# Kernel tuning notes

Hardware: AMD Instinct MI355X
Metric: run time of the kernel (lower is better)

Reference implementation:

```python
import jax, jax.numpy as jnp
import numpy as np
from jax import lax

GRID_SIZE = 5
SPLINE_ORDER = 3
N_COEF = GRID_SIZE + SPLINE_ORDER  # 8 b-spline basis functions per input
GRID_LO, GRID_HI = -1.0, 1.0


def _grid():
    h = (GRID_HI - GRID_LO) / GRID_SIZE
    return jnp.arange(-SPLINE_ORDER, GRID_SIZE + SPLINE_ORDER + 1, dtype=jnp.float32) * h + GRID_LO


def _bsplines(x):
    # x: [..., in] -> [..., in, N_COEF] via Cox-de Boor recursion (efficient-kan)
    grid = _grid()
    x = x[..., None]
    bases = ((x >= grid[:-1]) & (x < grid[1:])).astype(x.dtype)
    for j in range(1, SPLINE_ORDER + 1):
        bases = ((x - grid[:-(j + 1)]) / (grid[j:-1] - grid[:-(j + 1)]) * bases[..., :-1]
                 + (grid[j + 1:] - x) / (grid[j + 1:] - grid[1:-j]) * bases[..., 1:])
    return bases


def _kan_linear(x, base_w, spline_w):
    # x: [..., in]; base_w: [out, in]; spline_w: [out, in, N_COEF]
    base = jax.nn.silu(x) @ base_w.T
    b = _bsplines(x).reshape(x.shape[:-1] + (-1,))  # [..., in*N_COEF]
    return base + b @ spline_w.reshape(spline_w.shape[0], -1).T


def _kan_conv(x, base_w, spline_w):
    # x: [B, C, H, W]; 3x3 valid KAN convolution
    patches = lax.conv_general_dilated_patches(x, (3, 3), (1, 1), 'VALID')  # [B, C*9, H-2, W-2]
    p = patches.transpose(0, 2, 3, 1)  # [B, Ho, Wo, C*9]
    out = _kan_linear(p, base_w, spline_w)  # [B, Ho, Wo, out]
    return out.transpose(0, 3, 1, 2)


def _maxpool2(x):
    return lax.reduce_window(x, -jnp.inf, lax.max, (1, 1, 2, 2), (1, 1, 2, 2), 'VALID')


def setup_inputs() -> dict:
    key = jax.random.key(0)
    ks = jax.random.split(key, 12)
    B = 2048
    x = jax.random.uniform(ks[0], (B, 1, 28, 28), dtype=jnp.float32)
    s = 0.1
    return {
        'x': x,
        'bw1': jax.random.normal(ks[1], (5, 9), dtype=jnp.float32) * s,
        'sw1': jax.random.normal(ks[2], (5, 9, N_COEF), dtype=jnp.float32) * s,
        'bw2': jax.random.normal(ks[3], (5, 45), dtype=jnp.float32) * s,
        'sw2': jax.random.normal(ks[4], (5, 45, N_COEF), dtype=jnp.float32) * s,
        'bw3': jax.random.normal(ks[5], (2, 45), dtype=jnp.float32) * s,
        'sw3': jax.random.normal(ks[6], (2, 45, N_COEF), dtype=jnp.float32) * s,
        'w1': jax.random.normal(ks[7], (500, 162), dtype=jnp.float32) * 0.05,
        'b1': jnp.zeros((500,), dtype=jnp.float32),
        'w2': jax.random.normal(ks[8], (10, 500), dtype=jnp.float32) * 0.05,
        'b2': jnp.zeros((10,), dtype=jnp.float32),
    }


def reference(x, bw1, sw1, bw2, sw2, bw3, sw3, w1, b1, w2, b2):
    h = _kan_conv(x, bw1, sw1)       # [B, 5, 26, 26]
    h = _maxpool2(h)                 # [B, 5, 13, 13]
    h = _kan_conv(h, bw2, sw2)       # [B, 5, 11, 11]
    h = _kan_conv(h, bw3, sw3)       # [B, 2, 9, 9]
    h = h.reshape(h.shape[0], -1)    # [B, 162]
    h = jax.nn.relu(h @ w1.T + b1)   # [B, 500]
    return h @ w2.T + b2             # [B, 10]
```

## Files before the change

kernel.cpp:

```cpp
#include <hip/hip_runtime.h>


typedef _Float16 h2 __attribute__((ext_vector_type(2)));

__device__ __forceinline__ h2 u2h(unsigned int u) {
  union { unsigned int x; h2 h; } v; v.x = u; return v.h;
}
__device__ __forceinline__ unsigned short f2h_bits(float x) {
  union { _Float16 h; unsigned short u; } v; v.h = (_Float16)x; return v.u;
}
__device__ __forceinline__ float h2f(unsigned short u) {
  union { unsigned short u; _Float16 h; } v; v.u = u; return (float)v.h;
}
__device__ __forceinline__ unsigned int pack2h(float a, float b) {
  return (unsigned int)f2h_bits(a) | ((unsigned int)f2h_bits(b) << 16);
}
__device__ __forceinline__ float fdot2(h2 a, h2 b, float c) {
  return __builtin_amdgcn_fdot2(a, b, c, false);
}

__device__ __forceinline__ void featurize_regs(float v, uint4& bs, float& silu) {
  silu = v / (1.0f + __expf(-v));
  bs.x = 0u; bs.y = 0u; bs.z = 0u; bs.w = 0u;
  float u = fmaf(v, 2.5f, 5.5f);
  if (u >= 0.0f && u < 11.0f) {
    float tf = floorf(u);
    float f = u - tf, f2 = f * f, f3 = f2 * f, om = 1.0f - f;
    const float c6 = 1.0f / 6.0f;
    float w0 = om * om * om * c6;
    float w1 = (3.0f * f3 - 6.0f * f2 + 4.0f) * c6;
    float w2 = (-3.0f * f3 + 3.0f * f2 + 3.0f * f + 1.0f) * c6;
    float w3 = f3 * c6;
    unsigned long long w01 =
        (unsigned long long)f2h_bits(w0) |
        ((unsigned long long)f2h_bits(w1) << 16) |
        ((unsigned long long)f2h_bits(w2) << 32) |
        ((unsigned long long)f2h_bits(w3) << 48);
    int t = (int)tf;
    int s = 16 * t - 48;
    unsigned long long lo, hi;
    if (s >= 0) {
      lo = (s < 64) ? (w01 << s) : 0ull;
      hi = (s == 0) ? 0ull : ((s < 64) ? (w01 >> (64 - s)) : (w01 << (s - 64)));
    } else {
      lo = w01 >> (-s);
      hi = 0ull;
    }
    bs.x = (unsigned int)lo; bs.y = (unsigned int)(lo >> 32);
    bs.z = (unsigned int)hi; bs.w = (unsigned int)(hi >> 32);
  }
}

template <int OB, int NO>
__device__ __forceinline__ void conv2_accum(
    const uint4* bas, const unsigned short* slu16,
    const unsigned int* __restrict__ V2s, const float* __restrict__ V2b,
    int y0, int x0, float (&acc)[NO]) {
  #pragma unroll 1
  for (int cky = 0; cky < 15; ++cky) {
    int c = cky / 3, ky = cky - c * 3;
    int ba0 = c * 169 + (y0 + ky) * 13 + x0;
    uint4 q00 = bas[ba0], q01 = bas[ba0 + 1], q02 = bas[ba0 + 2];
    float s00 = h2f(slu16[ba0]), s01 = h2f(slu16[ba0 + 1]), s02 = h2f(slu16[ba0 + 2]);
    uint4 wq[3 * NO]; float wb[3 * NO];
    const uint4* wp4 = (const uint4*)(V2s + cky * 60);
    const float* bp  = V2b + cky * 15;
    #pragma unroll
    for (int kx = 0; kx < 3; ++kx)
      #pragma unroll
      for (int j = 0; j < NO; ++j) {
        wq[kx * NO + j] = wp4[kx * 5 + OB + j];
        wb[kx * NO + j] = bp[kx * 5 + OB + j];
      }
    #pragma unroll
    for (int kx = 0; kx < 3; ++kx) {
      uint4 q = (kx == 0) ? q00 : ((kx == 1) ? q01 : q02);
      float sl = (kx == 0) ? s00 : ((kx == 1) ? s01 : s02);
      h2 a0 = u2h(q.x), a1 = u2h(q.y), a2 = u2h(q.z), a3 = u2h(q.w);
      #pragma unroll
      for (int j = 0; j < NO; ++j) {
        uint4 w = wq[kx * NO + j];
        float a = acc[j];
        a = fdot2(a0, u2h(w.x), a);
        a = fdot2(a1, u2h(w.y), a);
        a = fdot2(a2, u2h(w.z), a);
        a = fdot2(a3, u2h(w.w), a);
        acc[j] = fmaf(sl, wb[kx * NO + j], a);
      }
    }
  }
}

__global__ __launch_bounds__(256) void k_prep(
    const float* __restrict__ bw1, const float* __restrict__ sw1,
    const float* __restrict__ bw2, const float* __restrict__ sw2,
    const float* __restrict__ bw3, const float* __restrict__ sw3,
    const float* __restrict__ w1, const float* __restrict__ w2,
    unsigned int* __restrict__ V1s, float* __restrict__ V1b,
    unsigned int* __restrict__ V2s, float* __restrict__ V2b,
    unsigned int* __restrict__ V3s, float* __restrict__ V3b,
    unsigned int* __restrict__ W1p4, float* __restrict__ W2p) {
  int t = blockIdx.x * 256 + threadIdx.x;
  if (t < 180) {
    int p = t & 3, o = (t >> 2) % 5, in = t / 20;
    V1s[t] = pack2h(sw1[(o * 9 + in) * 8 + 2 * p], sw1[(o * 9 + in) * 8 + 2 * p + 1]);
  }
  if (t < 45)  { int o = t % 5, in = t / 5; V1b[t] = bw1[o * 9 + in]; }
  if (t < 900) {
    int p = t & 3, o = (t >> 2) % 5, in = t / 20;
    V2s[t] = pack2h(sw2[(o * 45 + in) * 8 + 2 * p], sw2[(o * 45 + in) * 8 + 2 * p + 1]);
  }
  if (t < 225) { int o = t % 5, in = t / 5; V2b[t] = bw2[o * 45 + in]; }
  if (t < 360) {
    int p = t & 3, o = (t >> 2) & 1, in = t / 8;
    V3s[t] = pack2h(sw3[(o * 45 + in) * 8 + 2 * p], sw3[(o * 45 + in) * 8 + 2 * p + 1]);
  }
  if (t < 90)  { int o = t % 2, in = t / 2; V3b[t] = bw3[o * 45 + in]; }
  if (t < 43008) {
    int j = t & 3, o = (t >> 2) & 511, g = t >> 11;
    int kp = g * 4 + j;
    W1p4[t] = (o < 500 && kp < 81)
                  ? pack2h(w1[o * 162 + 2 * kp], w1[o * 162 + 2 * kp + 1])
                  : 0u;
  }
  if (t < 5120) {
    int o = t >> 9, k = t & 511;
    W2p[t] = (k < 500) ? w2[o * 500 + k] : 0.0f;
  }
}

__global__ __launch_bounds__(256, 8) void k_fused(
    const float* __restrict__ x,
    const unsigned int* __restrict__ V1s, const float* __restrict__ V1b,
    const unsigned int* __restrict__ V2s, const float* __restrict__ V2b,
    const unsigned int* __restrict__ V3s, const float* __restrict__ V3b,
    const unsigned int* __restrict__ W1p4, const float* __restrict__ W2p,
    const float* __restrict__ b1, const float* __restrict__ b2,
    float* __restrict__ out) {
  __shared__ uint4 bas[845];
  __shared__ unsigned short slu16[848];
  __shared__ float red[40];
  float*        basF = (float*)bas;
  float*        h3f  = basF + 2048;
  unsigned int* hpk  = (unsigned int*)basF + 2560;
  const int b = blockIdx.x;
  const int tid = threadIdx.x;

  #pragma unroll 1
  for (int l = tid; l < 784; l += 256) {
    uint4 bs; float sl;
    featurize_regs(x[b * 784 + l], bs, sl);
    bas[l] = bs; slu16[l] = f2h_bits(sl);
  }
  __syncthreads();

  float h1v[5];
  if (tid < 169) {
    int py = tid / 13, px = tid % 13;
    int r0 = py * 2, c0 = px * 2;
    float wacc[4][5];
    #pragma unroll
    for (int wi = 0; wi < 4; ++wi)
      #pragma unroll
      for (int o = 0; o < 5; ++o) wacc[wi][o] = 0.0f;
    #pragma unroll
    for (int r = 0; r < 4; ++r) {
      uint4 q[4]; float sl[4];
      #pragma unroll
      for (int c = 0; c < 4; ++c) {
        q[c]  = bas[(r0 + r) * 28 + c0 + c];
        sl[c] = h2f(slu16[(r0 + r) * 28 + c0 + c]);
      }
      #pragma unroll
      for (int c = 0; c < 4; ++c) {
        h2 a0 = u2h(q[c].x), a1 = u2h(q[c].y), a2 = u2h(q[c].z), a3 = u2h(q[c].w);
        #pragma unroll
        for (int dy = 0; dy < 2; ++dy) {
          #pragma unroll
          for (int dx = 0; dx < 2; ++dx) {
            int ky = r - dy, kx = c - dx;
            if (ky >= 0 && ky < 3 && kx >= 0 && kx < 3) {
              const unsigned int* wp = V1s + (ky * 3 + kx) * 20;
              const float* bp = V1b + (ky * 3 + kx) * 5;
              #pragma unroll
              for (int o = 0; o < 5; ++o) {
                float acc = wacc[dy * 2 + dx][o];
                acc = fdot2(a0, u2h(wp[o * 4 + 0]), acc);
                acc = fdot2(a1, u2h(wp[o * 4 + 1]), acc);
                acc = fdot2(a2, u2h(wp[o * 4 + 2]), acc);
                acc = fdot2(a3, u2h(wp[o * 4 + 3]), acc);
                wacc[dy * 2 + dx][o] = fmaf(sl[c], bp[o], acc);
              }
            }
          }
        }
      }
    }
    #pragma unroll
    for (int o = 0; o < 5; ++o)
      h1v[o] = fmaxf(fmaxf(wacc[0][o], wacc[1][o]),
                     fmaxf(wacc[2][o], wacc[3][o]));
  }
  __syncthreads();
  if (tid < 169) {
    #pragma unroll
    for (int o = 0; o < 5; ++o) {
      uint4 bs; float sl;
      featurize_regs(h1v[o], bs, sl);
      bas[o * 169 + tid] = bs; slu16[o * 169 + tid] = f2h_bits(sl);
    }
  }
  __syncthreads();

  int og = __builtin_amdgcn_readfirstlane(tid >> 7);
  int p2 = tid & 127;
  float acc2a[3] = {0.0f, 0.0f, 0.0f};
  float acc2b[2] = {0.0f, 0.0f};
  {
    int pc = (p2 < 121) ? p2 : 120;
    int y0 = pc / 11, x0 = pc % 11;
    if (og == 0) conv2_accum<0, 3>(bas, slu16, V2s, V2b, y0, x0, acc2a);
    else         conv2_accum<3, 2>(bas, slu16, V2s, V2b, y0, x0, acc2b);
  }
  __syncthreads();
  if (p2 < 121) {
    if (og == 0) {
      #pragma unroll
      for (int j = 0; j < 3; ++j) {
        uint4 bs; float sl;
        featurize_regs(acc2a[j], bs, sl);
        bas[j * 121 + p2] = bs; slu16[j * 121 + p2] = f2h_bits(sl);
      }
    } else {
      #pragma unroll
      for (int j = 0; j < 2; ++j) {
        uint4 bs; float sl;
        featurize_regs(acc2b[j], bs, sl);
        bas[(3 + j) * 121 + p2] = bs; slu16[(3 + j) * 121 + p2] = f2h_bits(sl);
      }
    }
  }
  __syncthreads();

  float acc3 = 0.0f;
  {
    int ou = og;
    int pc = (p2 < 81) ? p2 : 80;
    int y0 = pc / 9, x0 = pc % 9;
    #pragma unroll 1
    for (int cky = 0; cky < 15; ++cky) {
      int c = cky / 3, ky = cky - c * 3;
      int ba0 = c * 121 + (y0 + ky) * 11 + x0;
      uint4 q00 = bas[ba0], q01 = bas[ba0 + 1], q02 = bas[ba0 + 2];
      float s00 = h2f(slu16[ba0]), s01 = h2f(slu16[ba0 + 1]), s02 = h2f(slu16[ba0 + 2]);
      uint4 wq[3]; float wb[3];
      const uint4* wp4 = (const uint4*)(V3s + cky * 24);
      const float* bp  = V3b + cky * 6;
      #pragma unroll
      for (int kx = 0; kx < 3; ++kx) {
        wq[kx] = wp4[kx * 2 + ou];
        wb[kx] = bp[kx * 2 + ou];
      }
      #pragma unroll
      for (int kx = 0; kx < 3; ++kx) {
        uint4 q = (kx == 0) ? q00 : ((kx == 1) ? q01 : q02);
        float sl = (kx == 0) ? s00 : ((kx == 1) ? s01 : s02);
        h2 a0 = u2h(q.x), a1 = u2h(q.y), a2 = u2h(q.z), a3 = u2h(q.w);
        uint4 w = wq[kx];
        float a = acc3;
        a = fdot2(a0, u2h(w.x), a);
        a = fdot2(a1, u2h(w.y), a);
        a = fdot2(a2, u2h(w.z), a);
        a = fdot2(a3, u2h(w.w), a);
        acc3 = fmaf(sl, wb[kx], a);
      }
    }
  }
  __syncthreads();
  if (p2 < 81) h3f[og * 81 + p2] = acc3;
  __syncthreads();
  if (tid < 84)
    hpk[tid] = (tid < 81) ? pack2h(h3f[2 * tid], h3f[2 * tid + 1]) : 0u;
  __syncthreads();

  float fa[2] = {0.0f, 0.0f};
  {
    const uint4* hp4 = (const uint4*)hpk;
    const uint4* wbase = (const uint4*)W1p4 + tid;
    uint4 wA[2], wB[2];
    #pragma unroll
    for (int i = 0; i < 2; ++i) wA[i] = wbase[i * 256];
    #pragma unroll 1
    for (int g = 0; g < 21; g += 2) {
      if (g + 1 < 21) {
        const uint4* p = wbase + (g + 1) * 512;
        #pragma unroll
        for (int i = 0; i < 2; ++i) wB[i] = p[i * 256];
      }
      {
        uint4 hk = hp4[g];
        #pragma unroll
        for (int i = 0; i < 2; ++i) {
          float a = fa[i];
          a = fdot2(u2h(hk.x), u2h(wA[i].x), a);
          a = fdot2(u2h(hk.y), u2h(wA[i].y), a);
          a = fdot2(u2h(hk.z), u2h(wA[i].z), a);
          a = fdot2(u2h(hk.w), u2h(wA[i].w), a);
          fa[i] = a;
        }
      }
      if (g + 2 < 21) {
        const uint4* p = wbase + (g + 2) * 512;
        #pragma unroll
        for (int i = 0; i < 2; ++i) wA[i] = p[i * 256];
      }
      if (g + 1 < 21) {
        uint4 hk = hp4[g + 1];
        #pragma unroll
        for (int i = 0; i < 2; ++i) {
          float a = fa[i];
          a = fdot2(u2h(hk.x), u2h(wB[i].x), a);
          a = fdot2(u2h(hk.y), u2h(wB[i].y), a);
          a = fdot2(u2h(hk.z), u2h(wB[i].z), a);
          a = fdot2(u2h(hk.w), u2h(wB[i].w), a);
          fa[i] = a;
        }
      }
    }
  }
  #pragma unroll
  for (int i = 0; i < 2; ++i) {
    int o = tid + 256 * i;
    float bb = (o < 500) ? b1[o] : 0.0f;
    float v = fa[i] + bb;
    basF[o] = (v > 0.0f && o < 500) ? v : 0.0f;
  }
  __syncthreads();

  float acc10[10];
  {
    float2 ha = ((const float2*)basF)[tid];
    #pragma unroll
    for (int o = 0; o < 10; ++o) {
      float2 w = ((const float2*)&W2p[o * 512])[tid];
      acc10[o] = ha.x * w.x + ha.y * w.y;
    }
  }
  #pragma unroll
  for (int off = 32; off > 0; off >>= 1) {
    #pragma unroll
    for (int o = 0; o < 10; ++o) acc10[o] += __shfl_down(acc10[o], off);
  }
  if ((tid & 63) == 0) {
    int wid = tid >> 6;
    #pragma unroll
    for (int o = 0; o < 10; ++o) red[wid * 10 + o] = acc10[o];
  }
  __syncthreads();
  if (tid < 10)
    out[b * 10 + tid] = red[tid] + red[10 + tid] + red[20 + tid] + red[30 + tid] + b2[tid];
}

extern "C" void kernel_launch(void* const* d_in, const int* in_sizes, int n_in,
                              void* d_out, int out_size, void* d_ws, size_t ws_size,
                              hipStream_t stream) {
  (void)in_sizes; (void)n_in; (void)out_size; (void)ws_size;
  const float* x   = (const float*)d_in[0];
  const float* bw1 = (const float*)d_in[1];
  const float* sw1 = (const float*)d_in[2];
  const float* bw2 = (const float*)d_in[3];
  const float* sw2 = (const float*)d_in[4];
  const float* bw3 = (const float*)d_in[5];
  const float* sw3 = (const float*)d_in[6];
  const float* w1  = (const float*)d_in[7];
  const float* b1  = (const float*)d_in[8];
  const float* w2  = (const float*)d_in[9];
  const float* b2  = (const float*)d_in[10];
  float* out = (float*)d_out;

  char* ws = (char*)d_ws;
  unsigned int* V1s  = (unsigned int*)(ws);
  float*        V1b  = (float*)(ws + 768);
  unsigned int* V2s  = (unsigned int*)(ws + 1024);
  float*        V2b  = (float*)(ws + 4672);
  unsigned int* V3s  = (unsigned int*)(ws + 5632);
  float*        V3b  = (float*)(ws + 7168);
  float*        W2p  = (float*)(ws + 7680);
  unsigned int* W1p4 = (unsigned int*)(ws + 28672);

  k_prep<<<168, 256, 0, stream>>>(bw1, sw1, bw2, sw2, bw3, sw3, w1, w2,
                                  V1s, V1b, V2s, V2b, V3s, V3b, W1p4, W2p);
  k_fused<<<2048, 256, 0, stream>>>(x, V1s, V1b, V2s, V2b, V3s, V3b,
                                    W1p4, W2p, b1, b2, out);
}
```

Measured before the change: 129.1 us.

## Process two images per block and stage KAN conv weights in LDS

Each block now handles two images with 512 threads, and the conv weight tables for all three KAN layers are copied once per block into shared memory. Inner loops then read them from LDS instead of global/scalar memory. The first-layer feature map is stored with even and odd columns split apart, so each pool thread's four column reads are contiguous, likely to cut bank conflicts. Weight loads in conv2 and conv3 are moved inside the kx loop to lower register pressure. In exchange, shared memory per block roughly doubles, which may limit occupancy. Launch bounds of 512 with 8 blocks per CU also constrain registers.

```diff
diff --git a/kernel.cpp b/kernel.cpp
--- a/kernel.cpp
+++ b/kernel.cpp
@@ -54,7 +54,7 @@
 template <int OB, int NO>
 __device__ __forceinline__ void conv2_accum(
     const uint4* bas, const unsigned short* slu16,
-    const unsigned int* __restrict__ V2s, const float* __restrict__ V2b,
+    const unsigned int* wV2s, const float* wV2b,
     int y0, int x0, float (&acc)[NO]) {
   #pragma unroll 1
   for (int cky = 0; cky < 15; ++cky) {
@@ -62,30 +62,28 @@
     int ba0 = c * 169 + (y0 + ky) * 13 + x0;
     uint4 q00 = bas[ba0], q01 = bas[ba0 + 1], q02 = bas[ba0 + 2];
     float s00 = h2f(slu16[ba0]), s01 = h2f(slu16[ba0 + 1]), s02 = h2f(slu16[ba0 + 2]);
-    uint4 wq[3 * NO]; float wb[3 * NO];
-    const uint4* wp4 = (const uint4*)(V2s + cky * 60);
-    const float* bp  = V2b + cky * 15;
-    #pragma unroll
-    for (int kx = 0; kx < 3; ++kx)
+    const uint4* wp4 = (const uint4*)(wV2s + cky * 60);
+    const float* bp  = wV2b + cky * 15;
+    #pragma unroll
+    for (int kx = 0; kx < 3; ++kx) {
+      uint4 wq[NO]; float wb[NO];
       #pragma unroll
       for (int j = 0; j < NO; ++j) {
-        wq[kx * NO + j] = wp4[kx * 5 + OB + j];
-        wb[kx * NO + j] = bp[kx * 5 + OB + j];
-      }
-    #pragma unroll
-    for (int kx = 0; kx < 3; ++kx) {
+        wq[j] = wp4[kx * 5 + OB + j];
+        wb[j] = bp[kx * 5 + OB + j];
+      }
       uint4 q = (kx == 0) ? q00 : ((kx == 1) ? q01 : q02);
       float sl = (kx == 0) ? s00 : ((kx == 1) ? s01 : s02);
       h2 a0 = u2h(q.x), a1 = u2h(q.y), a2 = u2h(q.z), a3 = u2h(q.w);
       #pragma unroll
       for (int j = 0; j < NO; ++j) {
-        uint4 w = wq[kx * NO + j];
+        uint4 w = wq[j];
         float a = acc[j];
         a = fdot2(a0, u2h(w.x), a);
         a = fdot2(a1, u2h(w.y), a);
         a = fdot2(a2, u2h(w.z), a);
         a = fdot2(a3, u2h(w.w), a);
-        acc[j] = fmaf(sl, wb[kx * NO + j], a);
+        acc[j] = fmaf(sl, wb[j], a);
       }
     }
   }
@@ -129,7 +127,7 @@
   }
 }
 
-__global__ __launch_bounds__(256, 8) void k_fused(
+__global__ __launch_bounds__(512, 8) void k_fused(
     const float* __restrict__ x,
     const unsigned int* __restrict__ V1s, const float* __restrict__ V1b,
     const unsigned int* __restrict__ V2s, const float* __restrict__ V2b,
@@ -137,27 +135,49 @@
     const unsigned int* __restrict__ W1p4, const float* __restrict__ W2p,
     const float* __restrict__ b1, const float* __restrict__ b2,
     float* __restrict__ out) {
-  __shared__ uint4 bas[845];
-  __shared__ unsigned short slu16[848];
-  __shared__ float red[40];
-  float*        basF = (float*)bas;
-  float*        h3f  = basF + 2048;
-  unsigned int* hpk  = (unsigned int*)basF + 2560;
-  const int b = blockIdx.x;
+  __shared__ uint4 bas[2][845];
+  __shared__ unsigned short slu16[2][848];
+  __shared__ float red[2][40];
+  __shared__ __align__(16) unsigned int wV1s[180];
+  __shared__ float wV1b[45];
+  __shared__ __align__(16) unsigned int wV2s[900];
+  __shared__ float wV2b[225];
+  __shared__ __align__(16) unsigned int wV3s[360];
+  __shared__ float wV3b[90];
+
   const int tid = threadIdx.x;
+  const int h   = tid >> 8;
+  const int t   = tid & 255;
+
+  uint4*          bas_h = bas[h];
+  unsigned short* slu_h = slu16[h];
+  float*          basF  = (float*)bas_h;
+  float*          h3f   = basF + 2048;
+  unsigned int*   hpk   = (unsigned int*)basF + 2560;
+  const int img = blockIdx.x * 2 + h;
+
+  if (tid < 180) wV1s[tid] = V1s[tid];
+  if (tid < 45)  wV1b[tid] = V1b[tid];
+  #pragma unroll
+  for (int i = tid; i < 900; i += 512) wV2s[i] = V2s[i];
+  if (tid < 225) wV2b[tid] = V2b[tid];
+  if (tid < 360) wV3s[tid] = V3s[tid];
+  if (tid < 90)  wV3b[tid] = V3b[tid];
 
   #pragma unroll 1
-  for (int l = tid; l < 784; l += 256) {
+  for (int l = t; l < 784; l += 256) {
     uint4 bs; float sl;
-    featurize_regs(x[b * 784 + l], bs, sl);
-    bas[l] = bs; slu16[l] = f2h_bits(sl);
+    featurize_regs(x[img * 784 + l], bs, sl);
+    int y = l / 28, xx = l - y * 28;
+    int idx = y * 28 + ((xx & 1) ? 14 : 0) + (xx >> 1);
+    bas_h[idx] = bs; slu_h[idx] = f2h_bits(sl);
   }
   __syncthreads();
 
   float h1v[5];
-  if (tid < 169) {
-    int py = tid / 13, px = tid % 13;
-    int r0 = py * 2, c0 = px * 2;
+  if (t < 169) {
+    int py = t / 13, px = t % 13;
+    int r0 = py * 2;
     float wacc[4][5];
     #pragma unroll
     for (int wi = 0; wi < 4; ++wi)
@@ -168,8 +188,9 @@
       uint4 q[4]; float sl[4];
       #pragma unroll
       for (int c = 0; c < 4; ++c) {
-        q[c]  = bas[(r0 + r) * 28 + c0 + c];
-        sl[c] = h2f(slu16[(r0 + r) * 28 + c0 + c]);
+        int idx = (r0 + r) * 28 + ((c & 1) ? 14 : 0) + px + (c >> 1);
+        q[c]  = bas_h[idx];
+        sl[c] = h2f(slu_h[idx]);
       }
       #pragma unroll
       for (int c = 0; c < 4; ++c) {
@@ -180,15 +201,16 @@
           for (int dx = 0; dx < 2; ++dx) {
             int ky = r - dy, kx = c - dx;
             if (ky >= 0 && ky < 3 && kx >= 0 && kx < 3) {
-              const unsigned int* wp = V1s + (ky * 3 + kx) * 20;
-              const float* bp = V1b + (ky * 3 + kx) * 5;
+              const uint4* wp4 = (const uint4*)(wV1s + (ky * 3 + kx) * 20);
+              const float* bp  = wV1b + (ky * 3 + kx) * 5;
               #pragma unroll
               for (int o = 0; o < 5; ++o) {
+                uint4 w = wp4[o];
                 float acc = wacc[dy * 2 + dx][o];
-                acc = fdot2(a0, u2h(wp[o * 4 + 0]), acc);
-                acc = fdot2(a1, u2h(wp[o * 4 + 1]), acc);
-                acc = fdot2(a2, u2h(wp[o * 4 + 2]), acc);
-                acc = fdot2(a3, u2h(wp[o * 4 + 3]), acc);
+                acc = fdot2(a0, u2h(w.x), acc);
+                acc = fdot2(a1, u2h(w.y), acc);
+                acc = fdot2(a2, u2h(w.z), acc);
+                acc = fdot2(a3, u2h(w.w), acc);
                 wacc[dy * 2 + dx][o] = fmaf(sl[c], bp[o], acc);
               }
             }
@@ -202,25 +224,25 @@
                      fmaxf(wacc[2][o], wacc[3][o]));
   }
   __syncthreads();
-  if (tid < 169) {
+  if (t < 169) {
     #pragma unroll
     for (int o = 0; o < 5; ++o) {
       uint4 bs; float sl;
       featurize_regs(h1v[o], bs, sl);
-      bas[o * 169 + tid] = bs; slu16[o * 169 + tid] = f2h_bits(sl);
-    }
-  }
-  __syncthreads();
-
-  int og = __builtin_amdgcn_readfirstlane(tid >> 7);
-  int p2 = tid & 127;
+      bas_h[o * 169 + t] = bs; slu_h[o * 169 + t] = f2h_bits(sl);
+    }
+  }
+  __syncthreads();
+
+  int og = __builtin_amdgcn_readfirstlane(t >> 7);
+  int p2 = t & 127;
   float acc2a[3] = {0.0f, 0.0f, 0.0f};
   float acc2b[2] = {0.0f, 0.0f};
   {
     int pc = (p2 < 121) ? p2 : 120;
     int y0 = pc / 11, x0 = pc % 11;
-    if (og == 0) conv2_accum<0, 3>(bas, slu16, V2s, V2b, y0, x0, acc2a);
-    else         conv2_accum<3, 2>(bas, slu16, V2s, V2b, y0, x0, acc2b);
+    if (og == 0) conv2_accum<0, 3>(bas_h, slu_h, wV2s, wV2b, y0, x0, acc2a);
+    else         conv2_accum<3, 2>(bas_h, slu_h, wV2s, wV2b, y0, x0, acc2b);
   }
   __syncthreads();
   if (p2 < 121) {
@@ -229,14 +251,14 @@
       for (int j = 0; j < 3; ++j) {
         uint4 bs; float sl;
         featurize_regs(acc2a[j], bs, sl);
-        bas[j * 121 + p2] = bs; slu16[j * 121 + p2] = f2h_bits(sl);
+        bas_h[j * 121 + p2] = bs; slu_h[j * 121 + p2] = f2h_bits(sl);
       }
     } else {
       #pragma unroll
       for (int j = 0; j < 2; ++j) {
         uint4 bs; float sl;
         featurize_regs(acc2b[j], bs, sl);
-        bas[(3 + j) * 121 + p2] = bs; slu16[(3 + j) * 121 + p2] = f2h_bits(sl);
+        bas_h[(3 + j) * 121 + p2] = bs; slu_h[(3 + j) * 121 + p2] = f2h_bits(sl);
       }
     }
   }
@@ -251,42 +273,37 @@
     for (int cky = 0; cky < 15; ++cky) {
       int c = cky / 3, ky = cky - c * 3;
       int ba0 = c * 121 + (y0 + ky) * 11 + x0;
-      uint4 q00 = bas[ba0], q01 = bas[ba0 + 1], q02 = bas[ba0 + 2];
-      float s00 = h2f(slu16[ba0]), s01 = h2f(slu16[ba0 + 1]), s02 = h2f(slu16[ba0 + 2]);
-      uint4 wq[3]; float wb[3];
-      const uint4* wp4 = (const uint4*)(V3s + cky * 24);
-      const float* bp  = V3b + cky * 6;
+      uint4 q00 = bas_h[ba0], q01 = bas_h[ba0 + 1], q02 = bas_h[ba0 + 2];
+      float s00 = h2f(slu_h[ba0]), s01 = h2f(slu_h[ba0 + 1]), s02 = h2f(slu_h[ba0 + 2]);
+      const uint4* wp4 = (const uint4*)(wV3s + cky * 24);
+      const float* bp  = wV3b + cky * 6;
       #pragma unroll
       for (int kx = 0; kx < 3; ++kx) {
-        wq[kx] = wp4[kx * 2 + ou];
-        wb[kx] = bp[kx * 2 + ou];
-      }
-      #pragma unroll
-      for (int kx = 0; kx < 3; ++kx) {
+        uint4 w = wp4[kx * 2 + ou];
+        float wb = bp[kx * 2 + ou];
         uint4 q = (kx == 0) ? q00 : ((kx == 1) ? q01 : q02);
         float sl = (kx == 0) ? s00 : ((kx == 1) ? s01 : s02);
         h2 a0 = u2h(q.x), a1 = u2h(q.y), a2 = u2h(q.z), a3 = u2h(q.w);
-        uint4 w = wq[kx];
         float a = acc3;
         a = fdot2(a0, u2h(w.x), a);
         a = fdot2(a1, u2h(w.y), a);
         a = fdot2(a2, u2h(w.z), a);
         a = fdot2(a3, u2h(w.w), a);
-        acc3 = fmaf(sl, wb[kx], a);
+        acc3 = fmaf(sl, wb, a);
       }
     }
   }
   __syncthreads();
   if (p2 < 81) h3f[og * 81 + p2] = acc3;
   __syncthreads();
-  if (tid < 84)
-    hpk[tid] = (tid < 81) ? pack2h(h3f[2 * tid], h3f[2 * tid + 1]) : 0u;
+  if (t < 84)
+    hpk[t] = (t < 81) ? pack2h(h3f[2 * t], h3f[2 * t + 1]) : 0u;
   __syncthreads();
 
   float fa[2] = {0.0f, 0.0f};
   {
     const uint4* hp4 = (const uint4*)hpk;
-    const uint4* wbase = (const uint4*)W1p4 + tid;
+    const uint4* wbase = (const uint4*)W1p4 + t;
     uint4 wA[2], wB[2];
     #pragma unroll
     for (int i = 0; i < 2; ++i) wA[i] = wbase[i * 256];
@@ -330,7 +347,7 @@
   }
   #pragma unroll
   for (int i = 0; i < 2; ++i) {
-    int o = tid + 256 * i;
+    int o = t + 256 * i;
     float bb = (o < 500) ? b1[o] : 0.0f;
     float v = fa[i] + bb;
     basF[o] = (v > 0.0f && o < 500) ? v : 0.0f;
@@ -339,10 +356,10 @@
 
   float acc10[10];
   {
-    float2 ha = ((const float2*)basF)[tid];
+    float2 ha = ((const float2*)basF)[t];
     #pragma unroll
     for (int o = 0; o < 10; ++o) {
-      float2 w = ((const float2*)&W2p[o * 512])[tid];
+      float2 w = ((const float2*)&W2p[o * 512])[t];
       acc10[o] = ha.x * w.x + ha.y * w.y;
     }
   }
@@ -351,14 +368,15 @@
     #pragma unroll
     for (int o = 0; o < 10; ++o) acc10[o] += __shfl_down(acc10[o], off);
   }
-  if ((tid & 63) == 0) {
-    int wid = tid >> 6;
-    #pragma unroll
-    for (int o = 0; o < 10; ++o) red[wid * 10 + o] = acc10[o];
-  }
-  __syncthreads();
-  if (tid < 10)
-    out[b * 10 + tid] = red[tid] + red[10 + tid] + red[20 + tid] + red[30 + tid] + b2[tid];
+  if ((t & 63) == 0) {
+    int wid = t >> 6;
+    #pragma unroll
+    for (int o = 0; o < 10; ++o) red[h][wid * 10 + o] = acc10[o];
+  }
+  __syncthreads();
+  if (t < 10)
+    out[img * 10 + t] =
+        red[h][t] + red[h][10 + t] + red[h][20 + t] + red[h][30 + t] + b2[t];
 }
 
 extern "C" void kernel_launch(void* const* d_in, const int* in_sizes, int n_in,
@@ -390,6 +408,6 @@
 
   k_prep<<<168, 256, 0, stream>>>(bw1, sw1, bw2, sw2, bw3, sw3, w1, w2,
                                   V1s, V1b, V2s, V2b, V3s, V3b, W1p4, W2p);
-  k_fused<<<2048, 256, 0, stream>>>(x, V1s, V1b, V2s, V2b, V3s, V3b,
+  k_fused<<<1024, 512, 0, stream>>>(x, V1s, V1b, V2s, V2b, V3s, V3b,
                                     W1p4, W2p, b1, b2, out);
 }
```

Measured after the change: 293.8 us. 2.28x slower.
